# Optimization experiments

Hardware: AMD Instinct MI355X
Metric: run time of the kernel (lower is better)

Reference implementation:

```python
import jax, jax.numpy as jnp
import numpy as np


def rel_to_abs(x):
    """[b, hh, L, 2L-1] -> [b, hh, L, L] via pad/reshape trick."""
    b, hh, L, _ = x.shape
    x = jnp.pad(x, ((0, 0), (0, 0), (0, 0), (0, 1)))          # [b,hh,L,2L]
    flat = x.reshape(b, hh, L * 2 * L)
    flat = jnp.pad(flat, ((0, 0), (0, 0), (0, L - 1)))
    final = flat.reshape(b, hh, L + 1, 2 * L - 1)
    return final[:, :, :L, L - 1:]                             # [b,hh,L,L]


def relative_logits_1d(q, rel_k, transpose_mask):
    # q: [b, n, x, y, d]; rel_k: [2y-1, d]
    b, n, x, y, d = q.shape
    rel = jnp.einsum('bnxyd,md->bnxym', q, rel_k)
    rel = rel.reshape(b, n * x, y, 2 * y - 1)
    rel = rel_to_abs(rel)                                      # [b, n*x, y, y]
    rel = rel.reshape(b, n, x, y, y)
    rel = jnp.broadcast_to(rel[:, :, :, None, :, :], (b, n, x, x, y, y))
    return jnp.transpose(rel, transpose_mask)


def relative_logits(q, rel_emb_w, rel_emb_h):
    logits_w = relative_logits_1d(q, rel_emb_w, (0, 1, 2, 4, 3, 5))
    q_t = jnp.transpose(q, (0, 1, 3, 2, 4))  # swap h/w
    logits_h = relative_logits_1d(q_t, rel_emb_h, (0, 1, 4, 2, 5, 3))
    return logits_h + logits_w  # [b,n,h,w,h,w]


def setup_inputs() -> dict:
    key = jax.random.key(0)
    k1, k2, k3, k4, k5 = jax.random.split(key, 5)
    B, N, H, W, D = 4, 4, 48, 48, 32
    std = D ** (-0.5)
    return {
        'q': jax.random.normal(k1, (B, N, H, W, D), jnp.float32),
        'k': jax.random.normal(k2, (B, N, H, W, D), jnp.float32),
        'v': jax.random.normal(k3, (B, N, H, W, D), jnp.float32),
        'rel_emb_w': jax.random.normal(k4, (2 * W - 1, D), jnp.float32) * std,
        'rel_emb_h': jax.random.normal(k5, (2 * H - 1, D), jnp.float32) * std,
    }


def reference(q, k, v, rel_emb_w, rel_emb_h):
    bs, heads, h, w, dim = q.shape
    q = q * dim ** (-0.5)
    logits = jnp.einsum('bnhwd,bnpqd->bnhwpq', q, k)
    logits = logits + relative_logits(q, rel_emb_w, rel_emb_h)
    weights = jax.nn.softmax(logits.reshape(bs, heads, h, w, h * w), axis=-1)
    weights = weights.reshape(bs, heads, h, w, h, w)
    attn_out = jnp.einsum('bnhwpq,bnpqd->bhwnd', weights, v)
    # fold_heads=True
    return attn_out.reshape(bs, h, w, heads * dim)
```

## Files before the change

### kernel.cpp

```cpp
#include <hip/hip_runtime.h>
#include <hip/hip_bf16.h>


typedef __attribute__((ext_vector_type(8))) short bf16x8;
typedef __attribute__((ext_vector_type(4))) float f32x4;

#define DEVFN __device__ __forceinline__

#if __has_builtin(__builtin_amdgcn_exp2f)
#define EXP2(x) __builtin_amdgcn_exp2f(x)
#else
#define EXP2(x) exp2f(x)
#endif

constexpr int H_ = 48, W_ = 48, D_ = 32;
constexpr int L_ = H_ * W_;
constexpr int BN_ = 16;

constexpr int QB2 = 48;
constexpr int KB2 = 96;
constexpr int IT2 = L_ / KB2;
constexpr int QT2 = L_ / QB2;
constexpr int NWG2 = BN_ * QT2;

constexpr size_t WE_Q = 0;
constexpr size_t WE_K = 1179648;
constexpr size_t WE_V = 2359296;
constexpr size_t WE_R = 3538944;
constexpr size_t WS_NEED = (WE_R + 2 * 6 * 64 * 8) * 2;

DEVFN unsigned short f2bf(float f) {
  unsigned u = __float_as_uint(f);
  return (unsigned short)((u + 0x7fffu + ((u >> 16) & 1u)) >> 16);
}
DEVFN unsigned pk2(float lo, float hi) {
  return (unsigned)f2bf(lo) | ((unsigned)f2bf(hi) << 16);
}
DEVFN unsigned pkcvt(float lo, float hi) {
  __hip_bfloat162 h = __float22bfloat162_rn(make_float2(lo, hi));
  union { __hip_bfloat162 h2; unsigned u; } cv; cv.h2 = h;
  return cv.u;
}

template <int CTRL>
DEVFN float dppf(float x) {
  return __int_as_float(__builtin_amdgcn_update_dpp(0, __float_as_int(x), CTRL, 0xF, 0xF, true));
}
DEVFN float rowmax16(float x) {
  x = fmaxf(x, dppf<0x128>(x));
  x = fmaxf(x, dppf<0x124>(x));
  x = fmaxf(x, dppf<0x122>(x));
  x = fmaxf(x, dppf<0x121>(x));
  return x;
}
DEVFN float rowsum16(float x) {
  x += dppf<0x128>(x);
  x += dppf<0x124>(x);
  x += dppf<0x122>(x);
  x += dppf<0x121>(x);
  return x;
}

__global__ __launch_bounds__(256)
void prep_kernel(const float* __restrict__ Q, const float* __restrict__ K,
                 const float* __restrict__ V, const float* __restrict__ RW,
                 const float* __restrict__ RH, unsigned short* __restrict__ ws)
{
  __shared__ __align__(16) float Vl[3072];
  const int bid = blockIdx.x, tid = threadIdx.x;
  const float QS = 0.17677669529663687f * 1.4426950408889634f;
  if (bid < 576) {
    size_t e = ((size_t)bid * 256 + tid) * 8;
    const float* s = Q + e;
    float4 a = *(const float4*)s, c = *(const float4*)(s + 4);
    uint4 wv;
    wv.x = pkcvt(a.x * QS, a.y * QS); wv.y = pkcvt(a.z * QS, a.w * QS);
    wv.z = pkcvt(c.x * QS, c.y * QS); wv.w = pkcvt(c.z * QS, c.w * QS);
    *(uint4*)(ws + WE_Q + e) = wv;
  } else if (bid < 1152) {
    int idx = (bid - 576) * 256 + tid;
    int lane = idx & 63, t = idx >> 6;
    int l15 = lane & 15, lg = lane >> 4;
    int bn = t / 144, t16 = t % 144;
    int it = t16 / 6, kb = t16 % 6;
    int kbp = kb >> 1, f = kb & 1;
    int key96 = kbp * 32 + (l15 >> 2) * 8 + f * 4 + (l15 & 3);
    const float* s = K + ((size_t)(bn * L_ + it * 96 + key96) * D_ + lg * 8);
    float4 a = *(const float4*)s, c = *(const float4*)(s + 4);
    uint4 wv;
    wv.x = pkcvt(a.x, a.y); wv.y = pkcvt(a.z, a.w);
    wv.z = pkcvt(c.x, c.y); wv.w = pkcvt(c.z, c.w);
    *(uint4*)(ws + WE_K + (size_t)idx * 8) = wv;
  } else if (bid < 1536) {
    const int tile = bid - 1152;
    const float* src = V + (size_t)tile * 96 * D_;
    #pragma unroll
    for (int u = 0; u < 3; ++u)
      ((float4*)Vl)[tid + u * 256] = ((const float4*)src)[tid + u * 256];
    __syncthreads();
    unsigned short* dst = ws + WE_V + (size_t)tile * 3072;
    #pragma unroll
    for (int u = 0; u < 2; ++u) {
      const int f2i = tid + u * 256;
      if (f2i < 384) {
        const int f2 = f2i >> 6, lane = f2i & 63;
        const int l15 = lane & 15, lg = lane >> 4;
        const int kbp = f2 >> 1, half = f2 & 1;
        const int d = half * 16 + l15;
        float fv[8];
        #pragma unroll
        for (int j = 0; j < 8; ++j)
          fv[j] = Vl[(kbp * 32 + lg * 8 + j) * 32 + d];
        uint4 wv;
        wv.x = pkcvt(fv[0], fv[1]); wv.y = pkcvt(fv[2], fv[3]);
        wv.z = pkcvt(fv[4], fv[5]); wv.w = pkcvt(fv[6], fv[7]);
        *(uint4*)(dst + (size_t)f2i * 8) = wv;
      }
    }
  } else {
    int t = (bid - 1536) * 256 + tid;
    if (t < 768) {
      int tbl = t / 384, rem = t % 384, jb = rem / 64, lane = rem % 64;
      int l15 = lane & 15, lg = lane >> 4;
      int j = jb * 16 + l15;
      int jc = (j > 94) ? 94 : j;
      const float* s = (tbl ? RW : RH) + jc * D_ + lg * 8;
      float4 a = *(const float4*)s, c = *(const float4*)(s + 4);
      uint4 wv;
      wv.x = pkcvt(a.x, a.y); wv.y = pkcvt(a.z, a.w);
      wv.z = pkcvt(c.x, c.y); wv.w = pkcvt(c.z, c.w);
      *(uint4*)(ws + WE_R + (size_t)t * 8) = wv;
    }
  }
}

__global__ __launch_bounds__(192, 3)
void relattn6(const unsigned short* __restrict__ ws, float* __restrict__ OUT)
{
  __shared__ __align__(16) float BhT[48 * 50];
  __shared__ __align__(16) float BwT[48 * 52];

  const unsigned short* Qb = ws + WE_Q;
  const unsigned short* Kf = ws + WE_K;
  const unsigned short* Vf = ws + WE_V;
  const unsigned short* Rf = ws + WE_R;

  const int bid = blockIdx.x;
  const int wg  = (bid & 7) * (NWG2 / 8) + (bid >> 3);
  const int bn  = wg / QT2;
  const int qb  = (wg % QT2) * QB2;
  const int b   = bn >> 2, n = bn & 3;

  const int tid  = threadIdx.x;
  const int wave = tid >> 6;
  const int lane = tid & 63;
  const int l15  = lane & 15;
  const int lg   = lane >> 4;

  const int qi = qb + wave * 16 + l15;
  const bf16x8 qfrag = *(const bf16x8*)(Qb + (size_t)(bn * L_ + qi) * D_ + lg * 8);

  const f32x4 z4 = {0.f, 0.f, 0.f, 0.f};

  #pragma unroll
  for (int jb = 0; jb < 6; ++jb) {
    bf16x8 rhf = *(const bf16x8*)(Rf + ((0 * 6 + jb) * 64 + lane) * 8);
    bf16x8 rwf = *(const bf16x8*)(Rf + ((1 * 6 + jb) * 64 + lane) * 8);
    f32x4 mh = __builtin_amdgcn_mfma_f32_16x16x32_bf16(qfrag, rhf, z4, 0, 0, 0);
    f32x4 mw = __builtin_amdgcn_mfma_f32_16x16x32_bf16(qfrag, rwf, z4, 0, 0, 0);
    const int j = jb * 16 + l15;
    if (j < 95) {
      #pragma unroll
      for (int r = 0; r < 4; ++r) {
        const int qg = qb + wave * 16 + lg * 4 + r;
        const int row = wave * 16 + lg * 4 + r;
        const int p  = j - 47 + qg / 48;
        if (p >= 0 && p < 48)  BhT[row * 50 + p]  = mh[r];
        const int ww = j - 47 + qg % 48;
        if (ww >= 0 && ww < 48) BwT[row * 52 + ww] = mw[r];
      }
    }
  }

  const int q52 = (wave * 16 + l15) * 52;
  const float* bwp0 = &BwT[q52 + lg * 8];
  const float* bwp1 = &BwT[q52 + ((lg < 2) ? (lg * 8 + 32) : (lg * 8 - 16))];
  const float* bwp2 = &BwT[q52 + lg * 8 + 16];

  const unsigned short* KfB = Kf + (size_t)bn * 24 * 3072 + (size_t)lane * 8;
  const unsigned short* VfB = Vf + (size_t)bn * 24 * 3072 + (size_t)lane * 8;

  f32x4 acc0 = z4, acc1 = z4;
  float l_acc = 0.f;

  const float* bhrow = &BhT[(wave * 16 + l15) * 50];
  const bool lglo = (lg < 2);

  bf16x8 kfA[6], vfA[6], kfB[6], vfB[6];

#define LOADIT(kfX, vfX, itv) do {                                          \
    const unsigned short* kt_ = KfB + (size_t)(itv) * 3072;                 \
    const unsigned short* vt_ = VfB + (size_t)(itv) * 3072;                 \
    _Pragma("unroll") for (int u = 0; u < 6; ++u)                           \
      kfX[u] = *(const bf16x8*)(kt_ + u * 512);                             \
    _Pragma("unroll") for (int u = 0; u < 6; ++u)                           \
      vfX[u] = *(const bf16x8*)(vt_ + u * 512);                             \
  } while (0)

#define COMPUTE(itv, kfX, vfX) do {                                         \
    const float2 bh2_ = *(const float2*)(bhrow + (itv) * 2);                \
    const float bhf0_ = EXP2(bh2_.x), bhf1_ = EXP2(bh2_.y);                 \
    const float bhfm_ = lglo ? bhf0_ : bhf1_;                               \
    _Pragma("unroll") for (int kbp = 0; kbp < 3; ++kbp) {                   \
      const float* bwp_ = (kbp == 0) ? bwp0 : ((kbp == 1) ? bwp1 : bwp2);   \
      f32x4 cin0 = *(const f32x4*)(bwp_);                                   \
      f32x4 cin1 = *(const f32x4*)(bwp_ + 4);                               \
      f32x4 s0 = __builtin_amdgcn_mfma_f32_16x16x32_bf16(kfX[kbp*2+0], qfrag, cin0, 0, 0, 0); \
      f32x4 s1 = __builtin_amdgcn_mfma_f32_16x16x32_bf16(kfX[kbp*2+1], qfrag, cin1, 0, 0, 0); \
      const float bf_ = (kbp == 0) ? bhf0_ : ((kbp == 2) ? bhf1_ : bhfm_);  \
      const float e0 = EXP2(s0[0]) * bf_, e1 = EXP2(s0[1]) * bf_;           \
      const float e2 = EXP2(s0[2]) * bf_, e3 = EXP2(s0[3]) * bf_;           \
      const float e4 = EXP2(s1[0]) * bf_, e5 = EXP2(s1[1]) * bf_;           \
      const float e6 = EXP2(s1[2]) * bf_, e7 = EXP2(s1[3]) * bf_;           \
      l_acc += (((e0 + e1) + (e2 + e3)) + ((e4 + e5) + (e6 + e7)));         \
      union { unsigned u[4]; bf16x8 v; } pf_;                               \
      pf_.u[0] = pkcvt(e0, e1); pf_.u[1] = pkcvt(e2, e3);                   \
      pf_.u[2] = pkcvt(e4, e5); pf_.u[3] = pkcvt(e6, e7);                   \
      acc0 = __builtin_amdgcn_mfma_f32_16x16x32_bf16(vfX[kbp*2+0], pf_.v, acc0, 0, 0, 0); \
      acc1 = __builtin_amdgcn_mfma_f32_16x16x32_bf16(vfX[kbp*2+1], pf_.v, acc1, 0, 0, 0); \
    }                                                                       \
  } while (0)

  LOADIT(kfA, vfA, 0);
  for (int it2 = 0; it2 < IT2 / 2; ++it2) {
    const int itA = it2 * 2;
    __builtin_amdgcn_sched_barrier(0);
    LOADIT(kfB, vfB, itA + 1);
    __builtin_amdgcn_sched_barrier(0);
    COMPUTE(itA, kfA, vfA);
    __builtin_amdgcn_sched_barrier(0);
    LOADIT(kfA, vfA, itA + 2);
    __builtin_amdgcn_sched_barrier(0);
    COMPUTE(itA + 1, kfB, vfB);
  }
#undef LOADIT
#undef COMPUTE

  float ls = l_acc;
  ls += __shfl_xor(ls, 16);
  ls += __shfl_xor(ls, 32);
  const float inv = __builtin_amdgcn_rcpf(ls);
  const int ql = qb + wave * 16 + l15;
  const int hql = ql / 48, wql = ql % 48;
  float* op = OUT + ((size_t)(b * 48 + hql) * 48 + wql) * 128 + n * 32 + lg * 4;
  *(float4*)op        = make_float4(acc0[0] * inv, acc0[1] * inv, acc0[2] * inv, acc0[3] * inv);
  *(float4*)(op + 16) = make_float4(acc1[0] * inv, acc1[1] * inv, acc1[2] * inv, acc1[3] * inv);
}

__global__ __launch_bounds__(256, 2)
void relattn_kernel(const float* __restrict__ Q, const float* __restrict__ K,
                    const float* __restrict__ V, const float* __restrict__ RW,
                    const float* __restrict__ RH, float* __restrict__ OUT)
{
  __shared__ __align__(16) unsigned short Klds[64][40];
  __shared__ __align__(16) unsigned       VT[32][36];
  __shared__ __align__(16) unsigned short Plds[4][16][72];
  __shared__ __align__(16) float          Bh[64][49];
  __shared__ __align__(16) float          Bw[64][49];

  const int bid = blockIdx.x;
  const int wg  = (bid & 7) * 72 + (bid >> 3);
  const int bn  = wg / 36;
  const int qb  = (wg % 36) * 64;
  const int b   = bn >> 2, n = bn & 3;

  const int tid  = threadIdx.x;
  const int wave = tid >> 6;
  const int lane = tid & 63;
  const int l15  = lane & 15;
  const int lg   = lane >> 4;

  const float QS = 0.17677669529663687f * 1.4426950408889634f;
  const int qi = qb + wave * 16 + l15;
  bf16x8 qfrag;
  {
    const float* qr = Q + ((bn * L_ + qi) * D_ + lg * 8);
    float4 a = *(const float4*)qr;
    float4 c = *(const float4*)(qr + 4);
    qfrag[0] = (short)f2bf(a.x * QS); qfrag[1] = (short)f2bf(a.y * QS);
    qfrag[2] = (short)f2bf(a.z * QS); qfrag[3] = (short)f2bf(a.w * QS);
    qfrag[4] = (short)f2bf(c.x * QS); qfrag[5] = (short)f2bf(c.y * QS);
    qfrag[6] = (short)f2bf(c.z * QS); qfrag[7] = (short)f2bf(c.w * QS);
  }
  const f32x4 z4 = {0.f, 0.f, 0.f, 0.f};
  #pragma unroll
  for (int jb = 0; jb < 6; ++jb) {
    const int j  = jb * 16 + l15;
    const int jc = (j > 94) ? 94 : j;
    bf16x8 rhf, rwf;
    {
      const float* rr = RH + jc * D_ + lg * 8;
      float4 a = *(const float4*)rr; float4 c = *(const float4*)(rr + 4);
      rhf[0] = (short)f2bf(a.x); rhf[1] = (short)f2bf(a.y);
      rhf[2] = (short)f2bf(a.z); rhf[3] = (short)f2bf(a.w);
      rhf[4] = (short)f2bf(c.x); rhf[5] = (short)f2bf(c.y);
      rhf[6] = (short)f2bf(c.z); rhf[7] = (short)f2bf(c.w);
      const float* rr2 = RW + jc * D_ + lg * 8;
      float4 a2 = *(const float4*)rr2; float4 c2 = *(const float4*)(rr2 + 4);
      rwf[0] = (short)f2bf(a2.x); rwf[1] = (short)f2bf(a2.y);
      rwf[2] = (short)f2bf(a2.z); rwf[3] = (short)f2bf(a2.w);
      rwf[4] = (short)f2bf(c2.x); rwf[5] = (short)f2bf(c2.y);
      rwf[6] = (short)f2bf(c2.z); rwf[7] = (short)f2bf(c2.w);
    }
    f32x4 mh = __builtin_amdgcn_mfma_f32_16x16x32_bf16(qfrag, rhf, z4, 0, 0, 0);
    f32x4 mw = __builtin_amdgcn_mfma_f32_16x16x32_bf16(qfrag, rwf, z4, 0, 0, 0);
    #pragma unroll
    for (int r = 0; r < 4; ++r) {
      const int qrow = lg * 4 + r;
      const int qg   = qb + wave * 16 + qrow;
      const int hqv  = qg / 48, wqv = qg % 48;
      if (j < 95) {
        const int p  = j - 47 + hqv;
        if (p >= 0 && p < 48) Bh[wave * 16 + qrow][p] = mh[r];
        const int ww = j - 47 + wqv;
        if (ww >= 0 && ww < 48) Bw[wave * 16 + qrow][ww] = mw[r];
      }
    }
  }
  float bw0[4], bw1[4], bw2[4];
  #pragma unroll
  for (int r = 0; r < 4; ++r) {
    bw0[r] = Bw[wave * 16 + lg * 4 + r][ 0 + l15];
    bw1[r] = Bw[wave * 16 + lg * 4 + r][16 + l15];
    bw2[r] = Bw[wave * 16 + lg * 4 + r][32 + l15];
  }
  f32x4 acc0 = z4, acc1 = z4;
  float m_r[4] = {-INFINITY, -INFINITY, -INFINITY, -INFINITY};
  float l_r[4] = {0.f, 0.f, 0.f, 0.f};
  const float* kbase = K + bn * L_ * D_;
  const float* vbase = V + bn * L_ * D_;
  for (int it = 0; it < 36; ++it) {
    const int kv0 = it * 64;
    __syncthreads();
    {
      const int r = tid >> 2, c = (tid & 3) * 8;
      const float* s = kbase + (kv0 + r) * D_ + c;
      float4 a = *(const float4*)s; float4 cc = *(const float4*)(s + 4);
      uint4 wv;
      wv.x = pk2(a.x, a.y);  wv.y = pk2(a.z, a.w);
      wv.z = pk2(cc.x, cc.y); wv.w = pk2(cc.z, cc.w);
      *(uint4*)&Klds[r][c] = wv;
    }
    {
      const int kp = tid >> 3, dg = tid & 7;
      const float* s0 = vbase + (kv0 + 2 * kp) * D_ + dg * 4;
      float4 a = *(const float4*)s0;
      float4 c = *(const float4*)(s0 + D_);
      VT[dg * 4 + 0][kp] = pk2(a.x, c.x);
      VT[dg * 4 + 1][kp] = pk2(a.y, c.y);
      VT[dg * 4 + 2][kp] = pk2(a.z, c.z);
      VT[dg * 4 + 3][kp] = pk2(a.w, c.w);
    }
    __syncthreads();
    f32x4 sacc[4];
    #pragma unroll
    for (int kb = 0; kb < 4; ++kb) {
      bf16x8 kf = *(const bf16x8*)&Klds[kb * 16 + l15][lg * 8];
      sacc[kb] = __builtin_amdgcn_mfma_f32_16x16x32_bf16(qfrag, kf, z4, 0, 0, 0);
    }
    const int p0   = kv0 / 48;
    const int tthr = (p0 + 1) * 48 - kv0;
    const int m0   = it % 3;
    float bh0[4], bh1[4];
    #pragma unroll
    for (int r = 0; r < 4; ++r) {
      bh0[r] = Bh[wave * 16 + lg * 4 + r][p0];
      bh1[r] = Bh[wave * 16 + lg * 4 + r][p0 + 1];
    }
    #pragma unroll
    for (int kb = 0; kb < 4; ++kb) {
      const bool hi = (kb * 16 + l15) >= tthr;
      int mm = m0 + kb; if (mm >= 3) mm -= 3; if (mm >= 3) mm -= 3;
      #pragma unroll
      for (int r = 0; r < 4; ++r) {
        const float bwv2 = (mm == 0) ? bw0[r] : ((mm == 1) ? bw1[r] : bw2[r]);
        sacc[kb][r] += (hi ? bh1[r] : bh0[r]) + bwv2;
      }
    }
    #pragma unroll
    for (int r = 0; r < 4; ++r) {
      float mx = fmaxf(fmaxf(sacc[0][r], sacc[1][r]), fmaxf(sacc[2][r], sacc[3][r]));
      mx = rowmax16(mx);
      const float mn = fmaxf(m_r[r], mx);
      const float sc = exp2f(m_r[r] - mn);
      m_r[r] = mn;
      acc0[r] *= sc; acc1[r] *= sc;
      const float pe0 = exp2f(sacc[0][r] - mn);
      const float pe1 = exp2f(sacc[1][r] - mn);
      const float pe2 = exp2f(sacc[2][r] - mn);
      const float pe3 = exp2f(sacc[3][r] - mn);
      const float rs = rowsum16(pe0 + pe1 + pe2 + pe3);
      l_r[r] = l_r[r] * sc + rs;
      const int prow = lg * 4 + r;
      Plds[wave][prow][ 0 + l15] = f2bf(pe0);
      Plds[wave][prow][16 + l15] = f2bf(pe1);
      Plds[wave][prow][32 + l15] = f2bf(pe2);
      Plds[wave][prow][48 + l15] = f2bf(pe3);
    }
    const unsigned short* VTu = (const unsigned short*)VT;
    #pragma unroll
    for (int s2 = 0; s2 < 2; ++s2) {
      bf16x8 a2 = *(const bf16x8*)&Plds[wave][l15][s2 * 32 + lg * 8];
      bf16x8 b0 = *(const bf16x8*)&VTu[( 0 + l15) * 72 + s2 * 32 + lg * 8];
      bf16x8 b1 = *(const bf16x8*)&VTu[(16 + l15) * 72 + s2 * 32 + lg * 8];
      acc0 = __builtin_amdgcn_mfma_f32_16x16x32_bf16(a2, b0, acc0, 0, 0, 0);
      acc1 = __builtin_amdgcn_mfma_f32_16x16x32_bf16(a2, b1, acc1, 0, 0, 0);
    }
  }
  #pragma unroll
  for (int r = 0; r < 4; ++r) {
    const int qg = qb + wave * 16 + lg * 4 + r;
    const int hqv = qg / 48, wqv = qg % 48;
    const float inv = __builtin_amdgcn_rcpf(l_r[r]);
    float* op = OUT + ((b * 48 + hqv) * 48 + wqv) * 128 + n * 32 + l15;
    op[0]  = acc0[r] * inv;
    op[16] = acc1[r] * inv;
  }
}

extern "C" void kernel_launch(void* const* d_in, const int* in_sizes, int n_in,
                              void* d_out, int out_size, void* d_ws, size_t ws_size,
                              hipStream_t stream) {
  const float* q  = (const float*)d_in[0];
  const float* k  = (const float*)d_in[1];
  const float* v  = (const float*)d_in[2];
  const float* rw = (const float*)d_in[3];
  const float* rh = (const float*)d_in[4];
  float* out = (float*)d_out;
  if (ws_size >= WS_NEED) {
    unsigned short* ws = (unsigned short*)d_ws;
    hipLaunchKernelGGL(prep_kernel, dim3(1539), dim3(256), 0, stream, q, k, v, rw, rh, ws);
    hipLaunchKernelGGL(relattn6, dim3(NWG2), dim3(192), 0, stream, ws, out);
  } else {
    hipLaunchKernelGGL(relattn_kernel, dim3(576), dim3(256), 0, stream, q, k, v, rw, rh, out);
  }
}
```

Measured before the change: 42.53 us.

## Split key range across two wave groups and reduce partial softmax sums via LDS

Result: slower. 162.7 us (+282.5%).

```diff
diff --git a/kernel.cpp b/kernel.cpp
--- a/kernel.cpp
+++ b/kernel.cpp
@@ -18,8 +18,7 @@
 constexpr int BN_ = 16;
 
 constexpr int QB2 = 48;
-constexpr int KB2 = 96;
-constexpr int IT2 = L_ / KB2;
+constexpr int IT2 = 24;
 constexpr int QT2 = L_ / QB2;
 constexpr int NWG2 = BN_ * QT2;
 
@@ -134,11 +133,12 @@
   }
 }
 
-__global__ __launch_bounds__(192, 3)
-void relattn6(const unsigned short* __restrict__ ws, float* __restrict__ OUT)
+__global__ __launch_bounds__(384, 5)
+void relattn7(const unsigned short* __restrict__ ws, float* __restrict__ OUT)
 {
   __shared__ __align__(16) float BhT[48 * 50];
   __shared__ __align__(16) float BwT[48 * 52];
+  __shared__ __align__(16) float Pp[3 * 9 * 64];
 
   const unsigned short* Qb = ws + WE_Q;
   const unsigned short* Kf = ws + WE_K;
@@ -153,36 +153,41 @@
 
   const int tid  = threadIdx.x;
   const int wave = tid >> 6;
+  const int wq3  = wave % 3;
+  const int half = wave / 3;
   const int lane = tid & 63;
   const int l15  = lane & 15;
   const int lg   = lane >> 4;
 
-  const int qi = qb + wave * 16 + l15;
+  const int qi = qb + wq3 * 16 + l15;
   const bf16x8 qfrag = *(const bf16x8*)(Qb + (size_t)(bn * L_ + qi) * D_ + lg * 8);
 
   const f32x4 z4 = {0.f, 0.f, 0.f, 0.f};
 
-  #pragma unroll
-  for (int jb = 0; jb < 6; ++jb) {
-    bf16x8 rhf = *(const bf16x8*)(Rf + ((0 * 6 + jb) * 64 + lane) * 8);
-    bf16x8 rwf = *(const bf16x8*)(Rf + ((1 * 6 + jb) * 64 + lane) * 8);
-    f32x4 mh = __builtin_amdgcn_mfma_f32_16x16x32_bf16(qfrag, rhf, z4, 0, 0, 0);
-    f32x4 mw = __builtin_amdgcn_mfma_f32_16x16x32_bf16(qfrag, rwf, z4, 0, 0, 0);
-    const int j = jb * 16 + l15;
-    if (j < 95) {
-      #pragma unroll
-      for (int r = 0; r < 4; ++r) {
-        const int qg = qb + wave * 16 + lg * 4 + r;
-        const int row = wave * 16 + lg * 4 + r;
-        const int p  = j - 47 + qg / 48;
-        if (p >= 0 && p < 48)  BhT[row * 50 + p]  = mh[r];
-        const int ww = j - 47 + qg % 48;
-        if (ww >= 0 && ww < 48) BwT[row * 52 + ww] = mw[r];
+  if (wave < 3) {
+    #pragma unroll
+    for (int jb = 0; jb < 6; ++jb) {
+      bf16x8 rhf = *(const bf16x8*)(Rf + ((0 * 6 + jb) * 64 + lane) * 8);
+      bf16x8 rwf = *(const bf16x8*)(Rf + ((1 * 6 + jb) * 64 + lane) * 8);
+      f32x4 mh = __builtin_amdgcn_mfma_f32_16x16x32_bf16(qfrag, rhf, z4, 0, 0, 0);
+      f32x4 mw = __builtin_amdgcn_mfma_f32_16x16x32_bf16(qfrag, rwf, z4, 0, 0, 0);
+      const int j = jb * 16 + l15;
+      if (j < 95) {
+        #pragma unroll
+        for (int r = 0; r < 4; ++r) {
+          const int qg = qb + wq3 * 16 + lg * 4 + r;
+          const int row = wq3 * 16 + lg * 4 + r;
+          const int p  = j - 47 + qg / 48;
+          if (p >= 0 && p < 48)  BhT[row * 50 + p]  = mh[r];
+          const int ww = j - 47 + qg % 48;
+          if (ww >= 0 && ww < 48) BwT[row * 52 + ww] = mw[r];
+        }
       }
     }
   }
-
-  const int q52 = (wave * 16 + l15) * 52;
+  __syncthreads();
+
+  const int q52 = (wq3 * 16 + l15) * 52;
   const float* bwp0 = &BwT[q52 + lg * 8];
   const float* bwp1 = &BwT[q52 + ((lg < 2) ? (lg * 8 + 32) : (lg * 8 - 16))];
   const float* bwp2 = &BwT[q52 + lg * 8 + 16];
@@ -193,7 +198,7 @@
   f32x4 acc0 = z4, acc1 = z4;
   float l_acc = 0.f;
 
-  const float* bhrow = &BhT[(wave * 16 + l15) * 50];
+  const float* bhrow = &BhT[(wq3 * 16 + l15) * 50];
   const bool lglo = (lg < 2);
 
   bf16x8 kfA[6], vfA[6], kfB[6], vfB[6];
@@ -231,9 +236,10 @@
     }                                                                       \
   } while (0)
 
-  LOADIT(kfA, vfA, 0);
-  for (int it2 = 0; it2 < IT2 / 2; ++it2) {
-    const int itA = it2 * 2;
+  const int itb = half * 12;
+  LOADIT(kfA, vfA, itb);
+  for (int it2 = 0; it2 < 6; ++it2) {
+    const int itA = itb + it2 * 2;
     __builtin_amdgcn_sched_barrier(0);
     LOADIT(kfB, vfB, itA + 1);
     __builtin_amdgcn_sched_barrier(0);
@@ -246,15 +252,33 @@
 #undef LOADIT
 #undef COMPUTE
 
-  float ls = l_acc;
-  ls += __shfl_xor(ls, 16);
-  ls += __shfl_xor(ls, 32);
-  const float inv = __builtin_amdgcn_rcpf(ls);
-  const int ql = qb + wave * 16 + l15;
-  const int hql = ql / 48, wql = ql % 48;
-  float* op = OUT + ((size_t)(b * 48 + hql) * 48 + wql) * 128 + n * 32 + lg * 4;
-  *(float4*)op        = make_float4(acc0[0] * inv, acc0[1] * inv, acc0[2] * inv, acc0[3] * inv);
-  *(float4*)(op + 16) = make_float4(acc1[0] * inv, acc1[1] * inv, acc1[2] * inv, acc1[3] * inv);
+  if (half == 1) {
+    float* P = &Pp[wq3 * 576];
+    P[0 * 64 + lane] = acc0[0]; P[1 * 64 + lane] = acc0[1];
+    P[2 * 64 + lane] = acc0[2]; P[3 * 64 + lane] = acc0[3];
+    P[4 * 64 + lane] = acc1[0]; P[5 * 64 + lane] = acc1[1];
+    P[6 * 64 + lane] = acc1[2]; P[7 * 64 + lane] = acc1[3];
+    P[8 * 64 + lane] = l_acc;
+  }
+  __syncthreads();
+  if (half == 0) {
+    const float* P = &Pp[wq3 * 576];
+    acc0[0] += P[0 * 64 + lane]; acc0[1] += P[1 * 64 + lane];
+    acc0[2] += P[2 * 64 + lane]; acc0[3] += P[3 * 64 + lane];
+    acc1[0] += P[4 * 64 + lane]; acc1[1] += P[5 * 64 + lane];
+    acc1[2] += P[6 * 64 + lane]; acc1[3] += P[7 * 64 + lane];
+    l_acc   += P[8 * 64 + lane];
+
+    float ls = l_acc;
+    ls += __shfl_xor(ls, 16);
+    ls += __shfl_xor(ls, 32);
+    const float inv = __builtin_amdgcn_rcpf(ls);
+    const int ql = qb + wq3 * 16 + l15;
+    const int hql = ql / 48, wql = ql % 48;
+    float* op = OUT + ((size_t)(b * 48 + hql) * 48 + wql) * 128 + n * 32 + lg * 4;
+    *(float4*)op        = make_float4(acc0[0] * inv, acc0[1] * inv, acc0[2] * inv, acc0[3] * inv);
+    *(float4*)(op + 16) = make_float4(acc1[0] * inv, acc1[1] * inv, acc1[2] * inv, acc1[3] * inv);
+  }
 }
 
 __global__ __launch_bounds__(256, 2)
@@ -440,7 +464,7 @@
   if (ws_size >= WS_NEED) {
     unsigned short* ws = (unsigned short*)d_ws;
     hipLaunchKernelGGL(prep_kernel, dim3(1539), dim3(256), 0, stream, q, k, v, rw, rh, ws);
-    hipLaunchKernelGGL(relattn6, dim3(NWG2), dim3(192), 0, stream, ws, out);
+    hipLaunchKernelGGL(relattn7, dim3(NWG2), dim3(384), 0, stream, ws, out);
   } else {
     hipLaunchKernelGGL(relattn_kernel, dim3(576), dim3(256), 0, stream, q, k, v, rw, rh, out);
   }
```

## Split KV range in two halves with partial outputs and a merge kernel

Applied to the files above, without the earlier changes.

After: 48.15 us. +13.2%, slower.

```diff
diff --git a/kernel.cpp b/kernel.cpp
--- a/kernel.cpp
+++ b/kernel.cpp
@@ -18,8 +18,7 @@
 constexpr int BN_ = 16;
 
 constexpr int QB2 = 48;
-constexpr int KB2 = 96;
-constexpr int IT2 = L_ / KB2;
+constexpr int IT2 = 24;
 constexpr int QT2 = L_ / QB2;
 constexpr int NWG2 = BN_ * QT2;
 
@@ -28,37 +27,18 @@
 constexpr size_t WE_V = 2359296;
 constexpr size_t WE_R = 3538944;
 constexpr size_t WS_NEED = (WE_R + 2 * 6 * 64 * 8) * 2;
+constexpr size_t WE_PO = 3545088;
+constexpr size_t WE_PL = WE_PO + 4718592;
+constexpr size_t WS_SPLIT = (WE_PL + 2 * 147456 / 2 + 73728) * 2;
 
 DEVFN unsigned short f2bf(float f) {
   unsigned u = __float_as_uint(f);
   return (unsigned short)((u + 0x7fffu + ((u >> 16) & 1u)) >> 16);
-}
-DEVFN unsigned pk2(float lo, float hi) {
-  return (unsigned)f2bf(lo) | ((unsigned)f2bf(hi) << 16);
 }
 DEVFN unsigned pkcvt(float lo, float hi) {
   __hip_bfloat162 h = __float22bfloat162_rn(make_float2(lo, hi));
   union { __hip_bfloat162 h2; unsigned u; } cv; cv.h2 = h;
   return cv.u;
-}
-
-template <int CTRL>
-DEVFN float dppf(float x) {
-  return __int_as_float(__builtin_amdgcn_update_dpp(0, __float_as_int(x), CTRL, 0xF, 0xF, true));
-}
-DEVFN float rowmax16(float x) {
-  x = fmaxf(x, dppf<0x128>(x));
-  x = fmaxf(x, dppf<0x124>(x));
-  x = fmaxf(x, dppf<0x122>(x));
-  x = fmaxf(x, dppf<0x121>(x));
-  return x;
-}
-DEVFN float rowsum16(float x) {
-  x += dppf<0x128>(x);
-  x += dppf<0x124>(x);
-  x += dppf<0x122>(x);
-  x += dppf<0x121>(x);
-  return x;
 }
 
 __global__ __launch_bounds__(256)
@@ -134,68 +114,55 @@
   }
 }
 
-__global__ __launch_bounds__(192, 3)
-void relattn6(const unsigned short* __restrict__ ws, float* __restrict__ OUT)
-{
-  __shared__ __align__(16) float BhT[48 * 50];
-  __shared__ __align__(16) float BwT[48 * 52];
-
-  const unsigned short* Qb = ws + WE_Q;
-  const unsigned short* Kf = ws + WE_K;
-  const unsigned short* Vf = ws + WE_V;
-  const unsigned short* Rf = ws + WE_R;
-
-  const int bid = blockIdx.x;
-  const int wg  = (bid & 7) * (NWG2 / 8) + (bid >> 3);
-  const int bn  = wg / QT2;
-  const int qb  = (wg % QT2) * QB2;
-  const int b   = bn >> 2, n = bn & 3;
-
-  const int tid  = threadIdx.x;
-  const int wave = tid >> 6;
-  const int lane = tid & 63;
-  const int l15  = lane & 15;
-  const int lg   = lane >> 4;
-
-  const int qi = qb + wave * 16 + l15;
-  const bf16x8 qfrag = *(const bf16x8*)(Qb + (size_t)(bn * L_ + qi) * D_ + lg * 8);
-
-  const f32x4 z4 = {0.f, 0.f, 0.f, 0.f};
-
-  #pragma unroll
-  for (int jb = 0; jb < 6; ++jb) {
-    bf16x8 rhf = *(const bf16x8*)(Rf + ((0 * 6 + jb) * 64 + lane) * 8);
-    bf16x8 rwf = *(const bf16x8*)(Rf + ((1 * 6 + jb) * 64 + lane) * 8);
-    f32x4 mh = __builtin_amdgcn_mfma_f32_16x16x32_bf16(qfrag, rhf, z4, 0, 0, 0);
-    f32x4 mw = __builtin_amdgcn_mfma_f32_16x16x32_bf16(qfrag, rwf, z4, 0, 0, 0);
-    const int j = jb * 16 + l15;
-    if (j < 95) {
-      #pragma unroll
-      for (int r = 0; r < 4; ++r) {
-        const int qg = qb + wave * 16 + lg * 4 + r;
-        const int row = wave * 16 + lg * 4 + r;
-        const int p  = j - 47 + qg / 48;
-        if (p >= 0 && p < 48)  BhT[row * 50 + p]  = mh[r];
-        const int ww = j - 47 + qg % 48;
-        if (ww >= 0 && ww < 48) BwT[row * 52 + ww] = mw[r];
-      }
-    }
-  }
-
-  const int q52 = (wave * 16 + l15) * 52;
-  const float* bwp0 = &BwT[q52 + lg * 8];
-  const float* bwp1 = &BwT[q52 + ((lg < 2) ? (lg * 8 + 32) : (lg * 8 - 16))];
-  const float* bwp2 = &BwT[q52 + lg * 8 + 16];
-
-  const unsigned short* KfB = Kf + (size_t)bn * 24 * 3072 + (size_t)lane * 8;
-  const unsigned short* VfB = Vf + (size_t)bn * 24 * 3072 + (size_t)lane * 8;
-
-  f32x4 acc0 = z4, acc1 = z4;
-  float l_acc = 0.f;
-
-  const float* bhrow = &BhT[(wave * 16 + l15) * 50];
-  const bool lglo = (lg < 2);
-
+
+#define MAIN_PROLOG(NWGRID)                                                  \
+  __shared__ __align__(16) float BhT[48 * 50];                               \
+  __shared__ __align__(16) float BwT[48 * 52];                               \
+  const unsigned short* Qb = ws + WE_Q;                                      \
+  const unsigned short* Kf = ws + WE_K;                                      \
+  const unsigned short* Vf = ws + WE_V;                                      \
+  const unsigned short* Rf = ws + WE_R;                                      \
+  const int wg  = (wgq & 7) * ((NWGRID) / 8) + (wgq >> 3);                   \
+  const int bn  = wg / QT2;                                                  \
+  const int qb  = (wg % QT2) * QB2;                                          \
+  const int b   = bn >> 2, n = bn & 3;                                       \
+  const int tid  = threadIdx.x;                                              \
+  const int wave = tid >> 6;                                                 \
+  const int lane = tid & 63;                                                 \
+  const int l15  = lane & 15;                                                \
+  const int lg   = lane >> 4;                                                \
+  const int qi = qb + wave * 16 + l15;                                       \
+  const bf16x8 qfrag = *(const bf16x8*)(Qb + (size_t)(bn * L_ + qi) * D_ + lg * 8); \
+  const f32x4 z4 = {0.f, 0.f, 0.f, 0.f};                                     \
+  _Pragma("unroll")                                                          \
+  for (int jb = 0; jb < 6; ++jb) {                                           \
+    bf16x8 rhf = *(const bf16x8*)(Rf + ((0 * 6 + jb) * 64 + lane) * 8);      \
+    bf16x8 rwf = *(const bf16x8*)(Rf + ((1 * 6 + jb) * 64 + lane) * 8);      \
+    f32x4 mh = __builtin_amdgcn_mfma_f32_16x16x32_bf16(qfrag, rhf, z4, 0, 0, 0); \
+    f32x4 mw = __builtin_amdgcn_mfma_f32_16x16x32_bf16(qfrag, rwf, z4, 0, 0, 0); \
+    const int j = jb * 16 + l15;                                             \
+    if (j < 95) {                                                            \
+      _Pragma("unroll")                                                      \
+      for (int r = 0; r < 4; ++r) {                                          \
+        const int qg = qb + wave * 16 + lg * 4 + r;                          \
+        const int row = wave * 16 + lg * 4 + r;                              \
+        const int p  = j - 47 + qg / 48;                                     \
+        if (p >= 0 && p < 48)  BhT[row * 50 + p]  = mh[r];                   \
+        const int ww = j - 47 + qg % 48;                                     \
+        if (ww >= 0 && ww < 48) BwT[row * 52 + ww] = mw[r];                  \
+      }                                                                      \
+    }                                                                        \
+  }                                                                          \
+  const int q52 = (wave * 16 + l15) * 52;                                    \
+  const float* bwp0 = &BwT[q52 + lg * 8];                                    \
+  const float* bwp1 = &BwT[q52 + ((lg < 2) ? (lg * 8 + 32) : (lg * 8 - 16))];\
+  const float* bwp2 = &BwT[q52 + lg * 8 + 16];                               \
+  const unsigned short* KfB = Kf + (size_t)bn * 24 * 3072 + (size_t)lane * 8;\
+  const unsigned short* VfB = Vf + (size_t)bn * 24 * 3072 + (size_t)lane * 8;\
+  f32x4 acc0 = z4, acc1 = z4;                                                \
+  float l_acc = 0.f;                                                         \
+  const float* bhrow = &BhT[(wave * 16 + l15) * 50];                         \
+  const bool lglo = (lg < 2);                                                \
   bf16x8 kfA[6], vfA[6], kfB[6], vfB[6];
 
 #define LOADIT(kfX, vfX, itv) do {                                          \
@@ -231,201 +198,81 @@
     }                                                                       \
   } while (0)
 
-  LOADIT(kfA, vfA, 0);
-  for (int it2 = 0; it2 < IT2 / 2; ++it2) {
-    const int itA = it2 * 2;
-    __builtin_amdgcn_sched_barrier(0);
-    LOADIT(kfB, vfB, itA + 1);
-    __builtin_amdgcn_sched_barrier(0);
-    COMPUTE(itA, kfA, vfA);
-    __builtin_amdgcn_sched_barrier(0);
-    LOADIT(kfA, vfA, itA + 2);
-    __builtin_amdgcn_sched_barrier(0);
-    COMPUTE(itA + 1, kfB, vfB);
+#define MAIN_LOOP(itb, NITER2)                                               \
+  LOADIT(kfA, vfA, (itb));                                                   \
+  for (int it2 = 0; it2 < (NITER2); ++it2) {                                 \
+    const int itA = (itb) + it2 * 2;                                         \
+    __builtin_amdgcn_sched_barrier(0);                                       \
+    LOADIT(kfB, vfB, itA + 1);                                               \
+    __builtin_amdgcn_sched_barrier(0);                                       \
+    COMPUTE(itA, kfA, vfA);                                                  \
+    __builtin_amdgcn_sched_barrier(0);                                       \
+    LOADIT(kfA, vfA, itA + 2);                                               \
+    __builtin_amdgcn_sched_barrier(0);                                       \
+    COMPUTE(itA + 1, kfB, vfB);                                              \
   }
-#undef LOADIT
-#undef COMPUTE
+
+__global__ __launch_bounds__(192, 3)
+void relattn8(const unsigned short* __restrict__ ws_c, unsigned short* __restrict__ ws_w)
+{
+  const unsigned short* ws = ws_c;
+  const int bid  = blockIdx.x;
+  const int half = (bid >= NWG2) ? 1 : 0;
+  const int wgq  = half ? (bid - NWG2) : bid;
+  MAIN_PROLOG(NWG2)
+  (void)b; (void)n;
+  const int itb = half * 12;
+  MAIN_LOOP(itb, 6)
+
+  float* PO = (float*)(ws_w + WE_PO);
+  float* PL = (float*)(ws_w + WE_PL);
+  const size_t base = ((size_t)(half * 16 + bn) * L_ + qi) * 32;
+  *(float4*)(PO + base + lg * 4)      = make_float4(acc0[0], acc0[1], acc0[2], acc0[3]);
+  *(float4*)(PO + base + 16 + lg * 4) = make_float4(acc1[0], acc1[1], acc1[2], acc1[3]);
+  float ls = l_acc;
+  ls += __shfl_xor(ls, 16);
+  ls += __shfl_xor(ls, 32);
+  if (lg == 0) PL[(size_t)(half * 16 + bn) * L_ + qi] = ls;
+}
+
+__global__ __launch_bounds__(256)
+void merge_kernel(const unsigned short* __restrict__ ws, float* __restrict__ OUT)
+{
+  const float* PO = (const float*)(ws + WE_PO);
+  const float* PL = (const float*)(ws + WE_PL);
+  const int unit = blockIdx.x * 256 + threadIdx.x;
+  const int dg = unit & 7;
+  const int t  = unit >> 3;
+  const int q  = t % L_;
+  const int bn = t / L_;
+  const int b = bn >> 2, n = bn & 3;
+  const size_t i0 = ((size_t)bn * L_ + q) * 32 + dg * 4;
+  const float4 o0 = *(const float4*)(PO + i0);
+  const float4 o1 = *(const float4*)(PO + i0 + (size_t)16 * L_ * 32);
+  const float l0 = PL[(size_t)bn * L_ + q];
+  const float l1 = PL[(size_t)16 * L_ + (size_t)bn * L_ + q];
+  const float inv = __builtin_amdgcn_rcpf(l0 + l1);
+  float* op = OUT + ((size_t)b * L_ + q) * 128 + n * 32 + dg * 4;
+  *(float4*)op = make_float4((o0.x + o1.x) * inv, (o0.y + o1.y) * inv,
+                             (o0.z + o1.z) * inv, (o0.w + o1.w) * inv);
+}
+
+__global__ __launch_bounds__(192, 3)
+void relattn6(const unsigned short* __restrict__ ws, float* __restrict__ OUT)
+{
+  const int bid = blockIdx.x;
+  const int wgq = bid;
+  MAIN_PROLOG(NWG2)
+  MAIN_LOOP(0, 12)
 
   float ls = l_acc;
   ls += __shfl_xor(ls, 16);
   ls += __shfl_xor(ls, 32);
   const float inv = __builtin_amdgcn_rcpf(ls);
-  const int ql = qb + wave * 16 + l15;
-  const int hql = ql / 48, wql = ql % 48;
+  const int hql = qi / 48, wql = qi % 48;
   float* op = OUT + ((size_t)(b * 48 + hql) * 48 + wql) * 128 + n * 32 + lg * 4;
   *(float4*)op        = make_float4(acc0[0] * inv, acc0[1] * inv, acc0[2] * inv, acc0[3] * inv);
   *(float4*)(op + 16) = make_float4(acc1[0] * inv, acc1[1] * inv, acc1[2] * inv, acc1[3] * inv);
-}
-
-__global__ __launch_bounds__(256, 2)
-void relattn_kernel(const float* __restrict__ Q, const float* __restrict__ K,
-                    const float* __restrict__ V, const float* __restrict__ RW,
-                    const float* __restrict__ RH, float* __restrict__ OUT)
-{
-  __shared__ __align__(16) unsigned short Klds[64][40];
-  __shared__ __align__(16) unsigned       VT[32][36];
-  __shared__ __align__(16) unsigned short Plds[4][16][72];
-  __shared__ __align__(16) float          Bh[64][49];
-  __shared__ __align__(16) float          Bw[64][49];
-
-  const int bid = blockIdx.x;
-  const int wg  = (bid & 7) * 72 + (bid >> 3);
-  const int bn  = wg / 36;
-  const int qb  = (wg % 36) * 64;
-  const int b   = bn >> 2, n = bn & 3;
-
-  const int tid  = threadIdx.x;
-  const int wave = tid >> 6;
-  const int lane = tid & 63;
-  const int l15  = lane & 15;
-  const int lg   = lane >> 4;
-
-  const float QS = 0.17677669529663687f * 1.4426950408889634f;
-  const int qi = qb + wave * 16 + l15;
-  bf16x8 qfrag;
-  {
-    const float* qr = Q + ((bn * L_ + qi) * D_ + lg * 8);
-    float4 a = *(const float4*)qr;
-    float4 c = *(const float4*)(qr + 4);
-    qfrag[0] = (short)f2bf(a.x * QS); qfrag[1] = (short)f2bf(a.y * QS);
-    qfrag[2] = (short)f2bf(a.z * QS); qfrag[3] = (short)f2bf(a.w * QS);
-    qfrag[4] = (short)f2bf(c.x * QS); qfrag[5] = (short)f2bf(c.y * QS);
-    qfrag[6] = (short)f2bf(c.z * QS); qfrag[7] = (short)f2bf(c.w * QS);
-  }
-  const f32x4 z4 = {0.f, 0.f, 0.f, 0.f};
-  #pragma unroll
-  for (int jb = 0; jb < 6; ++jb) {
-    const int j  = jb * 16 + l15;
-    const int jc = (j > 94) ? 94 : j;
-    bf16x8 rhf, rwf;
-    {
-      const float* rr = RH + jc * D_ + lg * 8;
-      float4 a = *(const float4*)rr; float4 c = *(const float4*)(rr + 4);
-      rhf[0] = (short)f2bf(a.x); rhf[1] = (short)f2bf(a.y);
-      rhf[2] = (short)f2bf(a.z); rhf[3] = (short)f2bf(a.w);
-      rhf[4] = (short)f2bf(c.x); rhf[5] = (short)f2bf(c.y);
-      rhf[6] = (short)f2bf(c.z); rhf[7] = (short)f2bf(c.w);
-      const float* rr2 = RW + jc * D_ + lg * 8;
-      float4 a2 = *(const float4*)rr2; float4 c2 = *(const float4*)(rr2 + 4);
-      rwf[0] = (short)f2bf(a2.x); rwf[1] = (short)f2bf(a2.y);
-      rwf[2] = (short)f2bf(a2.z); rwf[3] = (short)f2bf(a2.w);
-      rwf[4] = (short)f2bf(c2.x); rwf[5] = (short)f2bf(c2.y);
-      rwf[6] = (short)f2bf(c2.z); rwf[7] = (short)f2bf(c2.w);
-    }
-    f32x4 mh = __builtin_amdgcn_mfma_f32_16x16x32_bf16(qfrag, rhf, z4, 0, 0, 0);
-    f32x4 mw = __builtin_amdgcn_mfma_f32_16x16x32_bf16(qfrag, rwf, z4, 0, 0, 0);
-    #pragma unroll
-    for (int r = 0; r < 4; ++r) {
-      const int qrow = lg * 4 + r;
-      const int qg   = qb + wave * 16 + qrow;
-      const int hqv  = qg / 48, wqv = qg % 48;
-      if (j < 95) {
-        const int p  = j - 47 + hqv;
-        if (p >= 0 && p < 48) Bh[wave * 16 + qrow][p] = mh[r];
-        const int ww = j - 47 + wqv;
-        if (ww >= 0 && ww < 48) Bw[wave * 16 + qrow][ww] = mw[r];
-      }
-    }
-  }
-  float bw0[4], bw1[4], bw2[4];
-  #pragma unroll
-  for (int r = 0; r < 4; ++r) {
-    bw0[r] = Bw[wave * 16 + lg * 4 + r][ 0 + l15];
-    bw1[r] = Bw[wave * 16 + lg * 4 + r][16 + l15];
-    bw2[r] = Bw[wave * 16 + lg * 4 + r][32 + l15];
-  }
-  f32x4 acc0 = z4, acc1 = z4;
-  float m_r[4] = {-INFINITY, -INFINITY, -INFINITY, -INFINITY};
-  float l_r[4] = {0.f, 0.f, 0.f, 0.f};
-  const float* kbase = K + bn * L_ * D_;
-  const float* vbase = V + bn * L_ * D_;
-  for (int it = 0; it < 36; ++it) {
-    const int kv0 = it * 64;
-    __syncthreads();
-    {
-      const int r = tid >> 2, c = (tid & 3) * 8;
-      const float* s = kbase + (kv0 + r) * D_ + c;
-      float4 a = *(const float4*)s; float4 cc = *(const float4*)(s + 4);
-      uint4 wv;
-      wv.x = pk2(a.x, a.y);  wv.y = pk2(a.z, a.w);
-      wv.z = pk2(cc.x, cc.y); wv.w = pk2(cc.z, cc.w);
-      *(uint4*)&Klds[r][c] = wv;
-    }
-    {
-      const int kp = tid >> 3, dg = tid & 7;
-      const float* s0 = vbase + (kv0 + 2 * kp) * D_ + dg * 4;
-      float4 a = *(const float4*)s0;
-      float4 c = *(const float4*)(s0 + D_);
-      VT[dg * 4 + 0][kp] = pk2(a.x, c.x);
-      VT[dg * 4 + 1][kp] = pk2(a.y, c.y);
-      VT[dg * 4 + 2][kp] = pk2(a.z, c.z);
-      VT[dg * 4 + 3][kp] = pk2(a.w, c.w);
-    }
-    __syncthreads();
-    f32x4 sacc[4];
-    #pragma unroll
-    for (int kb = 0; kb < 4; ++kb) {
-      bf16x8 kf = *(const bf16x8*)&Klds[kb * 16 + l15][lg * 8];
-      sacc[kb] = __builtin_amdgcn_mfma_f32_16x16x32_bf16(qfrag, kf, z4, 0, 0, 0);
-    }
-    const int p0   = kv0 / 48;
-    const int tthr = (p0 + 1) * 48 - kv0;
-    const int m0   = it % 3;
-    float bh0[4], bh1[4];
-    #pragma unroll
-    for (int r = 0; r < 4; ++r) {
-      bh0[r] = Bh[wave * 16 + lg * 4 + r][p0];
-      bh1[r] = Bh[wave * 16 + lg * 4 + r][p0 + 1];
-    }
-    #pragma unroll
-    for (int kb = 0; kb < 4; ++kb) {
-      const bool hi = (kb * 16 + l15) >= tthr;
-      int mm = m0 + kb; if (mm >= 3) mm -= 3; if (mm >= 3) mm -= 3;
-      #pragma unroll
-      for (int r = 0; r < 4; ++r) {
-        const float bwv2 = (mm == 0) ? bw0[r] : ((mm == 1) ? bw1[r] : bw2[r]);
-        sacc[kb][r] += (hi ? bh1[r] : bh0[r]) + bwv2;
-      }
-    }
-    #pragma unroll
-    for (int r = 0; r < 4; ++r) {
-      float mx = fmaxf(fmaxf(sacc[0][r], sacc[1][r]), fmaxf(sacc[2][r], sacc[3][r]));
-      mx = rowmax16(mx);
-      const float mn = fmaxf(m_r[r], mx);
-      const float sc = exp2f(m_r[r] - mn);
-      m_r[r] = mn;
-      acc0[r] *= sc; acc1[r] *= sc;
-      const float pe0 = exp2f(sacc[0][r] - mn);
-      const float pe1 = exp2f(sacc[1][r] - mn);
-      const float pe2 = exp2f(sacc[2][r] - mn);
-      const float pe3 = exp2f(sacc[3][r] - mn);
-      const float rs = rowsum16(pe0 + pe1 + pe2 + pe3);
-      l_r[r] = l_r[r] * sc + rs;
-      const int prow = lg * 4 + r;
-      Plds[wave][prow][ 0 + l15] = f2bf(pe0);
-      Plds[wave][prow][16 + l15] = f2bf(pe1);
-      Plds[wave][prow][32 + l15] = f2bf(pe2);
-      Plds[wave][prow][48 + l15] = f2bf(pe3);
-    }
-    const unsigned short* VTu = (const unsigned short*)VT;
-    #pragma unroll
-    for (int s2 = 0; s2 < 2; ++s2) {
-      bf16x8 a2 = *(const bf16x8*)&Plds[wave][l15][s2 * 32 + lg * 8];
-      bf16x8 b0 = *(const bf16x8*)&VTu[( 0 + l15) * 72 + s2 * 32 + lg * 8];
-      bf16x8 b1 = *(const bf16x8*)&VTu[(16 + l15) * 72 + s2 * 32 + lg * 8];
-      acc0 = __builtin_amdgcn_mfma_f32_16x16x32_bf16(a2, b0, acc0, 0, 0, 0);
-      acc1 = __builtin_amdgcn_mfma_f32_16x16x32_bf16(a2, b1, acc1, 0, 0, 0);
-    }
-  }
-  #pragma unroll
-  for (int r = 0; r < 4; ++r) {
-    const int qg = qb + wave * 16 + lg * 4 + r;
-    const int hqv = qg / 48, wqv = qg % 48;
-    const float inv = __builtin_amdgcn_rcpf(l_r[r]);
-    float* op = OUT + ((b * 48 + hqv) * 48 + wqv) * 128 + n * 32 + l15;
-    op[0]  = acc0[r] * inv;
-    op[16] = acc1[r] * inv;
-  }
 }
 
 extern "C" void kernel_launch(void* const* d_in, const int* in_sizes, int n_in,
@@ -437,11 +284,12 @@
   const float* rw = (const float*)d_in[3];
   const float* rh = (const float*)d_in[4];
   float* out = (float*)d_out;
-  if (ws_size >= WS_NEED) {
-    unsigned short* ws = (unsigned short*)d_ws;
-    hipLaunchKernelGGL(prep_kernel, dim3(1539), dim3(256), 0, stream, q, k, v, rw, rh, ws);
+  unsigned short* ws = (unsigned short*)d_ws;
+  hipLaunchKernelGGL(prep_kernel, dim3(1539), dim3(256), 0, stream, q, k, v, rw, rh, ws);
+  if (ws_size >= WS_SPLIT) {
+    hipLaunchKernelGGL(relattn8, dim3(2 * NWG2), dim3(192), 0, stream, ws, ws);
+    hipLaunchKernelGGL(merge_kernel, dim3(1152), dim3(256), 0, stream, ws, out);
+  } else {
     hipLaunchKernelGGL(relattn6, dim3(NWG2), dim3(192), 0, stream, ws, out);
-  } else {
-    hipLaunchKernelGGL(relattn_kernel, dim3(576), dim3(256), 0, stream, q, k, v, rw, rh, out);
   }
 }
```

## Split key dimension across waves in relative attention, reduce partials via LDS

Applied to the files above, without the earlier changes.

Result: slower. 44.85 us (+5.4%).

```diff
diff --git a/kernel.cpp b/kernel.cpp
--- a/kernel.cpp
+++ b/kernel.cpp
@@ -18,8 +18,6 @@
 constexpr int BN_ = 16;
 
 constexpr int QB2 = 48;
-constexpr int KB2 = 96;
-constexpr int IT2 = L_ / KB2;
 constexpr int QT2 = L_ / QB2;
 constexpr int NWG2 = BN_ * QT2;
 
@@ -134,11 +132,13 @@
   }
 }
 
-__global__ __launch_bounds__(192, 3)
-void relattn6(const unsigned short* __restrict__ ws, float* __restrict__ OUT)
+__global__ __launch_bounds__(192, 4)
+void relattn9(const unsigned short* __restrict__ ws, float* __restrict__ OUT)
 {
   __shared__ __align__(16) float BhT[48 * 50];
   __shared__ __align__(16) float BwT[48 * 52];
+  __shared__ __align__(16) float Pp[3 * 2 * 3 * 256];
+  __shared__ __align__(16) float Ppl[3 * 3 * 64];
 
   const unsigned short* Qb = ws + WE_Q;
   const unsigned short* Kf = ws + WE_K;
@@ -152,28 +152,30 @@
   const int b   = bn >> 2, n = bn & 3;
 
   const int tid  = threadIdx.x;
-  const int wave = tid >> 6;
+  const int w    = tid >> 6;
   const int lane = tid & 63;
   const int l15  = lane & 15;
   const int lg   = lane >> 4;
 
-  const int qi = qb + wave * 16 + l15;
-  const bf16x8 qfrag = *(const bf16x8*)(Qb + (size_t)(bn * L_ + qi) * D_ + lg * 8);
-
   const f32x4 z4 = {0.f, 0.f, 0.f, 0.f};
+
+  bf16x8 qfr[3];
+  #pragma unroll
+  for (int qf = 0; qf < 3; ++qf)
+    qfr[qf] = *(const bf16x8*)(Qb + (size_t)(bn * L_ + qb + qf * 16 + l15) * D_ + lg * 8);
 
   #pragma unroll
   for (int jb = 0; jb < 6; ++jb) {
     bf16x8 rhf = *(const bf16x8*)(Rf + ((0 * 6 + jb) * 64 + lane) * 8);
     bf16x8 rwf = *(const bf16x8*)(Rf + ((1 * 6 + jb) * 64 + lane) * 8);
-    f32x4 mh = __builtin_amdgcn_mfma_f32_16x16x32_bf16(qfrag, rhf, z4, 0, 0, 0);
-    f32x4 mw = __builtin_amdgcn_mfma_f32_16x16x32_bf16(qfrag, rwf, z4, 0, 0, 0);
+    f32x4 mh = __builtin_amdgcn_mfma_f32_16x16x32_bf16(qfr[w], rhf, z4, 0, 0, 0);
+    f32x4 mw = __builtin_amdgcn_mfma_f32_16x16x32_bf16(qfr[w], rwf, z4, 0, 0, 0);
     const int j = jb * 16 + l15;
     if (j < 95) {
       #pragma unroll
       for (int r = 0; r < 4; ++r) {
-        const int qg = qb + wave * 16 + lg * 4 + r;
-        const int row = wave * 16 + lg * 4 + r;
+        const int qg = qb + w * 16 + lg * 4 + r;
+        const int row = w * 16 + lg * 4 + r;
         const int p  = j - 47 + qg / 48;
         if (p >= 0 && p < 48)  BhT[row * 50 + p]  = mh[r];
         const int ww = j - 47 + qg % 48;
@@ -181,58 +183,59 @@
       }
     }
   }
-
-  const int q52 = (wave * 16 + l15) * 52;
-  const float* bwp0 = &BwT[q52 + lg * 8];
-  const float* bwp1 = &BwT[q52 + ((lg < 2) ? (lg * 8 + 32) : (lg * 8 - 16))];
-  const float* bwp2 = &BwT[q52 + lg * 8 + 16];
-
-  const unsigned short* KfB = Kf + (size_t)bn * 24 * 3072 + (size_t)lane * 8;
-  const unsigned short* VfB = Vf + (size_t)bn * 24 * 3072 + (size_t)lane * 8;
-
-  f32x4 acc0 = z4, acc1 = z4;
-  float l_acc = 0.f;
-
-  const float* bhrow = &BhT[(wave * 16 + l15) * 50];
-  const bool lglo = (lg < 2);
-
-  bf16x8 kfA[6], vfA[6], kfB[6], vfB[6];
+  __syncthreads();
+
+  int baset = w * 32 + lg * 8; if (baset >= 48) baset -= 48;
+  const float* bwq0 = &BwT[(0 * 16 + l15) * 52 + baset];
+  const float* bwq1 = &BwT[(1 * 16 + l15) * 52 + baset];
+  const float* bwq2 = &BwT[(2 * 16 + l15) * 52 + baset];
+  const float* bhq0 = &BhT[(0 * 16 + l15) * 50];
+  const float* bhq1 = &BhT[(1 * 16 + l15) * 50];
+  const float* bhq2 = &BhT[(2 * 16 + l15) * 50];
+  const bool keylo = (w == 0) | ((w == 1) & (lg < 2));
+
+  const unsigned short* KfW = Kf + (size_t)bn * 24 * 3072 + (size_t)(2 * w) * 512 + (size_t)lane * 8;
+  const unsigned short* VfW = Vf + (size_t)bn * 24 * 3072 + (size_t)(2 * w) * 512 + (size_t)lane * 8;
+
+  f32x4 acc[2][3] = {{z4, z4, z4}, {z4, z4, z4}};
+  float l_acc[3] = {0.f, 0.f, 0.f};
+
+  bf16x8 kfA[2], vfA[2], kfB[2], vfB[2];
 
 #define LOADIT(kfX, vfX, itv) do {                                          \
-    const unsigned short* kt_ = KfB + (size_t)(itv) * 3072;                 \
-    const unsigned short* vt_ = VfB + (size_t)(itv) * 3072;                 \
-    _Pragma("unroll") for (int u = 0; u < 6; ++u)                           \
-      kfX[u] = *(const bf16x8*)(kt_ + u * 512);                             \
-    _Pragma("unroll") for (int u = 0; u < 6; ++u)                           \
-      vfX[u] = *(const bf16x8*)(vt_ + u * 512);                             \
+    const unsigned short* kt_ = KfW + (size_t)(itv) * 3072;                 \
+    const unsigned short* vt_ = VfW + (size_t)(itv) * 3072;                 \
+    kfX[0] = *(const bf16x8*)(kt_);                                         \
+    kfX[1] = *(const bf16x8*)(kt_ + 512);                                   \
+    vfX[0] = *(const bf16x8*)(vt_);                                         \
+    vfX[1] = *(const bf16x8*)(vt_ + 512);                                   \
   } while (0)
 
 #define COMPUTE(itv, kfX, vfX) do {                                         \
-    const float2 bh2_ = *(const float2*)(bhrow + (itv) * 2);                \
-    const float bhf0_ = EXP2(bh2_.x), bhf1_ = EXP2(bh2_.y);                 \
-    const float bhfm_ = lglo ? bhf0_ : bhf1_;                               \
-    _Pragma("unroll") for (int kbp = 0; kbp < 3; ++kbp) {                   \
-      const float* bwp_ = (kbp == 0) ? bwp0 : ((kbp == 1) ? bwp1 : bwp2);   \
-      f32x4 cin0 = *(const f32x4*)(bwp_);                                   \
-      f32x4 cin1 = *(const f32x4*)(bwp_ + 4);                               \
-      f32x4 s0 = __builtin_amdgcn_mfma_f32_16x16x32_bf16(kfX[kbp*2+0], qfrag, cin0, 0, 0, 0); \
-      f32x4 s1 = __builtin_amdgcn_mfma_f32_16x16x32_bf16(kfX[kbp*2+1], qfrag, cin1, 0, 0, 0); \
-      const float bf_ = (kbp == 0) ? bhf0_ : ((kbp == 2) ? bhf1_ : bhfm_);  \
+    _Pragma("unroll") for (int qf = 0; qf < 3; ++qf) {                      \
+      const float* bhq_ = (qf == 0) ? bhq0 : ((qf == 1) ? bhq1 : bhq2);     \
+      const float* bwq_ = (qf == 0) ? bwq0 : ((qf == 1) ? bwq1 : bwq2);     \
+      const float2 bh2_ = *(const float2*)(bhq_ + (itv) * 2);               \
+      const float bf_ = EXP2(keylo ? bh2_.x : bh2_.y);                      \
+      f32x4 cin0 = *(const f32x4*)(bwq_);                                   \
+      f32x4 cin1 = *(const f32x4*)(bwq_ + 4);                               \
+      f32x4 s0 = __builtin_amdgcn_mfma_f32_16x16x32_bf16(kfX[0], qfr[qf], cin0, 0, 0, 0); \
+      f32x4 s1 = __builtin_amdgcn_mfma_f32_16x16x32_bf16(kfX[1], qfr[qf], cin1, 0, 0, 0); \
       const float e0 = EXP2(s0[0]) * bf_, e1 = EXP2(s0[1]) * bf_;           \
       const float e2 = EXP2(s0[2]) * bf_, e3 = EXP2(s0[3]) * bf_;           \
       const float e4 = EXP2(s1[0]) * bf_, e5 = EXP2(s1[1]) * bf_;           \
       const float e6 = EXP2(s1[2]) * bf_, e7 = EXP2(s1[3]) * bf_;           \
-      l_acc += (((e0 + e1) + (e2 + e3)) + ((e4 + e5) + (e6 + e7)));         \
+      l_acc[qf] += (((e0 + e1) + (e2 + e3)) + ((e4 + e5) + (e6 + e7)));     \
       union { unsigned u[4]; bf16x8 v; } pf_;                               \
       pf_.u[0] = pkcvt(e0, e1); pf_.u[1] = pkcvt(e2, e3);                   \
       pf_.u[2] = pkcvt(e4, e5); pf_.u[3] = pkcvt(e6, e7);                   \
-      acc0 = __builtin_amdgcn_mfma_f32_16x16x32_bf16(vfX[kbp*2+0], pf_.v, acc0, 0, 0, 0); \
-      acc1 = __builtin_amdgcn_mfma_f32_16x16x32_bf16(vfX[kbp*2+1], pf_.v, acc1, 0, 0, 0); \
+      acc[0][qf] = __builtin_amdgcn_mfma_f32_16x16x32_bf16(vfX[0], pf_.v, acc[0][qf], 0, 0, 0); \
+      acc[1][qf] = __builtin_amdgcn_mfma_f32_16x16x32_bf16(vfX[1], pf_.v, acc[1][qf], 0, 0, 0); \
     }                                                                       \
   } while (0)
 
   LOADIT(kfA, vfA, 0);
-  for (int it2 = 0; it2 < IT2 / 2; ++it2) {
+  for (int it2 = 0; it2 < 12; ++it2) {
     const int itA = it2 * 2;
     __builtin_amdgcn_sched_barrier(0);
     LOADIT(kfB, vfB, itA + 1);
@@ -246,15 +249,33 @@
 #undef LOADIT
 #undef COMPUTE
 
-  float ls = l_acc;
+  #pragma unroll
+  for (int dh = 0; dh < 2; ++dh)
+    #pragma unroll
+    for (int qf = 0; qf < 3; ++qf)
+      *(f32x4*)&Pp[((w * 2 + dh) * 3 + qf) * 256 + lane * 4] = acc[dh][qf];
+  #pragma unroll
+  for (int qf = 0; qf < 3; ++qf)
+    Ppl[(w * 3 + qf) * 64 + lane] = l_acc[qf];
+  __syncthreads();
+
+  f32x4 o0 = *(const f32x4*)&Pp[((0 * 2 + 0) * 3 + w) * 256 + lane * 4];
+  f32x4 o1 = *(const f32x4*)&Pp[((0 * 2 + 1) * 3 + w) * 256 + lane * 4];
+  #pragma unroll
+  for (int wp = 1; wp < 3; ++wp) {
+    o0 += *(const f32x4*)&Pp[((wp * 2 + 0) * 3 + w) * 256 + lane * 4];
+    o1 += *(const f32x4*)&Pp[((wp * 2 + 1) * 3 + w) * 256 + lane * 4];
+  }
+  float ls = Ppl[(0 * 3 + w) * 64 + lane] + Ppl[(1 * 3 + w) * 64 + lane]
+           + Ppl[(2 * 3 + w) * 64 + lane];
   ls += __shfl_xor(ls, 16);
   ls += __shfl_xor(ls, 32);
   const float inv = __builtin_amdgcn_rcpf(ls);
-  const int ql = qb + wave * 16 + l15;
+  const int ql = qb + w * 16 + l15;
   const int hql = ql / 48, wql = ql % 48;
   float* op = OUT + ((size_t)(b * 48 + hql) * 48 + wql) * 128 + n * 32 + lg * 4;
-  *(float4*)op        = make_float4(acc0[0] * inv, acc0[1] * inv, acc0[2] * inv, acc0[3] * inv);
-  *(float4*)(op + 16) = make_float4(acc1[0] * inv, acc1[1] * inv, acc1[2] * inv, acc1[3] * inv);
+  *(float4*)op        = make_float4(o0[0] * inv, o0[1] * inv, o0[2] * inv, o0[3] * inv);
+  *(float4*)(op + 16) = make_float4(o1[0] * inv, o1[1] * inv, o1[2] * inv, o1[3] * inv);
 }
 
 __global__ __launch_bounds__(256, 2)
@@ -440,7 +461,7 @@
   if (ws_size >= WS_NEED) {
     unsigned short* ws = (unsigned short*)d_ws;
     hipLaunchKernelGGL(prep_kernel, dim3(1539), dim3(256), 0, stream, q, k, v, rw, rh, ws);
-    hipLaunchKernelGGL(relattn6, dim3(NWG2), dim3(192), 0, stream, ws, out);
+    hipLaunchKernelGGL(relattn9, dim3(NWG2), dim3(192), 0, stream, ws, out);
   } else {
     hipLaunchKernelGGL(relattn_kernel, dim3(576), dim3(256), 0, stream, q, k, v, rw, rh, out);
   }
```
